# Optimization experiments

Hardware: AMD Instinct MI355X
Metric: run time of the kernel (lower is better)

## Reference

```python
import jax, jax.numpy as jnp
import numpy as np

L, D, H, DK, DV, VOCAB, PAD = 6, 512, 8, 64, 64, 10000, 0
B, S, NR = 32, 64, 196

def setup_inputs() -> dict:
    key = jax.random.key(0)
    ks = jax.random.split(key, 16)
    sd = 0.02
    emb = jax.random.normal(ks[0], (VOCAB, D), jnp.float32) * sd
    emb = emb.at[PAD].set(0.0)  # padding_idx row is zero in torch Embedding
    def w(k, shape):
        return jax.random.normal(k, shape, jnp.float32) * sd
    return {
        "x": jax.random.randint(ks[1], (B, S), 0, VOCAB),
        "K": jax.random.normal(ks[2], (B, NR, D), jnp.float32),
        "V": jax.random.normal(ks[3], (B, NR, D), jnp.float32),
        "g": jax.random.normal(ks[4], (B, D), jnp.float32),
        "batch_size": B,
        "emb": emb,
        "Wq_s": w(ks[5], (L, D, H * DK)),
        "Wk_s": w(ks[6], (L, D, H * DK)),
        "Wv_s": w(ks[7], (L, D, H * DV)),
        "Wo_s": w(ks[8], (L, H * DV, D)),
        "Wq_c": w(ks[9], (L, D, H * DK)),
        "Wg_c": w(ks[10], (L, D, H * DK)),
        "Wk_c": w(ks[11], (L, D, H * DK)),
        "Wv_c": w(ks[12], (L, D, H * DV)),
        "Wo_c": w(ks[13], (L, H * DV, D)),
        "Wf": w(ks[14], (D, VOCAB)),
        "bf": jnp.zeros((VOCAB,), jnp.float32),
    }

def positional_encoding(seq_len, d_model):
    pos = jnp.arange(seq_len, dtype=jnp.float32)[:, None]          # [S,1]
    j = jnp.arange(d_model // 2, dtype=jnp.float32)[None, :]       # [1,D/2]
    ang = pos / jnp.power(10000.0, 2.0 * j / d_model)              # [S,D/2]
    pe = jnp.stack([jnp.sin(ang), jnp.cos(ang)], axis=-1)          # [S,D/2,2]
    return pe.reshape(seq_len, d_model)

def attend(q, k, v, mask):
    # q:[B,Sq,H,DK] k:[B,Sk,H,DK] v:[B,Sk,H,DV]
    scores = jnp.einsum('bqhd,bkhd->bhqk', q, k) / jnp.sqrt(jnp.float32(DK))
    if mask is not None:
        scores = jnp.where(mask[None, None], scores, jnp.finfo(scores.dtype).min)
    attn = jax.nn.softmax(scores, axis=-1)
    return jnp.einsum('bhqk,bkhd->bqhd', attn, v)

def reference(x, K, V, g, batch_size, emb, Wq_s, Wk_s, Wv_s, Wo_s,
              Wq_c, Wg_c, Wk_c, Wv_c, Wo_c, Wf, bf):
    b, s = x.shape
    out = emb[x] + positional_encoding(s, D)[None]                 # [B,S,D]
    mask = jnp.tril(jnp.ones((s, s), bool))                        # causal: True = attend
    for l in range(L):
        # masked multi-head self-attention
        q = (out @ Wq_s[l]).reshape(b, s, H, DK)
        k = (out @ Wk_s[l]).reshape(b, s, H, DK)
        v = (out @ Wv_s[l]).reshape(b, s, H, DV)
        out = attend(q, k, v, mask).reshape(b, s, H * DV) @ Wo_s[l]
        # global-adaptive cross-attention: query conditioned on global feature g
        q = (out @ Wq_c[l] + (g @ Wg_c[l])[:, None, :]).reshape(b, s, H, DK)
        kk = (K @ Wk_c[l]).reshape(b, NR, H, DK)
        vv = (V @ Wv_c[l]).reshape(b, NR, H, DV)
        out = attend(q, kk, vv, None).reshape(b, s, H * DV) @ Wo_c[l]
    return jax.nn.softmax(out @ Wf + bf, axis=-1)                  # [B,S,VOCAB]
```

## Files before the change

### kernel.cpp

```cpp
#include <hip/hip_runtime.h>
#include <math.h>


#define S2 (512*512)
typedef unsigned short ushort_t;
typedef unsigned int u32;
typedef __attribute__((ext_vector_type(8))) short short8;
typedef __attribute__((ext_vector_type(4))) float f32x4;

__device__ __forceinline__ ushort_t f2b(float f) {
    union { float f; u32 u; } v; v.f = f;
    u32 r = (v.u + 0x7fffu + ((v.u >> 16) & 1u)) >> 16;
    return (ushort_t)r;
}
__device__ __forceinline__ float b2f(ushort_t u) {
    union { u32 u; float f; } v; v.u = ((u32)u) << 16; return v.f;
}
__device__ __forceinline__ void glds16(const void* g, void* l) {
    __builtin_amdgcn_global_load_lds((const __attribute__((address_space(1))) u32*)g,
                                     (__attribute__((address_space(3))) u32*)l,
                                     16, 0, 0);
}
__device__ __forceinline__ f32x4 mfma16(short8 a, short8 b, f32x4 c) {
    return __builtin_amdgcn_mfma_f32_16x16x32_bf16(a, b, c, 0, 0, 0);
}

__device__ __forceinline__ void tile128(
    const ushort_t* __restrict__ A, const ushort_t* __restrict__ B,
    ushort_t* __restrict__ Cp, int N, int K, const float* __restrict__ biasc,
    int m0, int n0, ushort_t* As, ushort_t* Bs, ushort_t* Cs)
{
    int t = threadIdx.x;
    int sr = t >> 2, sk = (t & 3) * 8;
    int wv = t >> 6, lane = t & 63;
    int wr = (wv >> 1) * 64, wc = (wv & 1) * 64;
    int lr = lane & 15, lq = lane >> 4;

    f32x4 acc[4][4];
#pragma unroll
    for (int i = 0; i < 4; ++i)
#pragma unroll
        for (int j = 0; j < 4; ++j) acc[i][j] = (f32x4){0.f, 0.f, 0.f, 0.f};

    for (int k0 = 0; k0 < K; k0 += 32) {
        glds16(A + (long)(m0 + sr) * K + k0 + sk,      (void*)(As + t * 8));
        glds16(A + (long)(m0 + sr + 64) * K + k0 + sk, (void*)(As + (t + 256) * 8));
        glds16(B + (long)(n0 + sr) * K + k0 + sk,      (void*)(Bs + t * 8));
        glds16(B + (long)(n0 + sr + 64) * K + k0 + sk, (void*)(Bs + (t + 256) * 8));
        __syncthreads();
        short8 af[4], bfr[4];
#pragma unroll
        for (int i = 0; i < 4; ++i)
            af[i] = *(const short8*)&As[(wr + i * 16 + lr) * 32 + lq * 8];
#pragma unroll
        for (int j = 0; j < 4; ++j)
            bfr[j] = *(const short8*)&Bs[(wc + j * 16 + lr) * 32 + lq * 8];
#pragma unroll
        for (int i = 0; i < 4; ++i)
#pragma unroll
            for (int j = 0; j < 4; ++j)
                acc[i][j] = mfma16(af[i], bfr[j], acc[i][j]);
        __syncthreads();
    }

    ushort_t* Cw = Cs + wv * 16 * 80;
#pragma unroll
    for (int i = 0; i < 4; ++i) {
#pragma unroll
        for (int j = 0; j < 4; ++j) {
            int colg = n0 + wc + j * 16 + lr;
            float bb = (biasc && colg < N) ? biasc[colg] : 0.f;
#pragma unroll
            for (int r = 0; r < 4; ++r)
                Cw[(lq * 4 + r) * 80 + j * 16 + lr] = f2b(acc[i][j][r] + bb);
        }
        __syncthreads();
#pragma unroll
        for (int rr = 0; rr < 2; ++rr) {
            int c = lane + 64 * rr;
            int row = c >> 3, g8 = c & 7;
            uint4 u = *(const uint4*)&Cw[row * 80 + g8 * 8];
            int colg = n0 + wc + g8 * 8;
            int rowg = m0 + wr + i * 16 + row;
            if (colg < N) *(uint4*)&Cp[(long)rowg * N + colg] = u;
        }
        __syncthreads();
    }
}

__global__ __launch_bounds__(256) void gemm_bt(
    const ushort_t* __restrict__ A, const ushort_t* __restrict__ B,
    ushort_t* __restrict__ C, int N, int K, const float* __restrict__ biasc)
{
    __shared__ ushort_t As[128 * 32], Bs[128 * 32];
    __shared__ __align__(16) ushort_t Cs[4 * 16 * 80];
    tile128(A, B, C, N, K, biasc, blockIdx.y * 128, blockIdx.x * 128, As, Bs, Cs);
}

__global__ __launch_bounds__(256) void fusew(
    const ushort_t* __restrict__ W8t, const ushort_t* __restrict__ Wo_sp,
    const ushort_t* __restrict__ Wo_cp, ushort_t* __restrict__ Fqc_t,
    ushort_t* __restrict__ Fqkv_t)
{
    __shared__ ushort_t As[128 * 32], Bs[128 * 32];
    __shared__ __align__(16) ushort_t Cs[4 * 16 * 80];
    int z = blockIdx.z;
    const ushort_t *A, *B; ushort_t* C;
    if (z < 6)      { A = W8t + (long)(24 + z) * S2; B = Wo_sp + (long)z * S2; C = Fqc_t + (long)z * S2; }
    else { int zz = z - 6, l = zz / 3, m = zz % 3;
           A = W8t + (long)(m * 6 + l + 1) * S2; B = Wo_cp + (long)l * S2; C = Fqkv_t + (long)zz * S2; }
    tile128(A, B, C, 512, 512, nullptr, blockIdx.y * 128, blockIdx.x * 128, As, Bs, Cs);
}

__global__ __launch_bounds__(256) void prep(
    const int* __restrict__ x, const float* __restrict__ emb,
    const float* __restrict__ Wq_s, const float* __restrict__ Wk_s,
    const float* __restrict__ Wv_s, const float* __restrict__ Wo_s,
    const float* __restrict__ Wq_c, const float* __restrict__ Wg_c,
    const float* __restrict__ Wk_c, const float* __restrict__ Wv_c,
    const float* __restrict__ Wo_c, const float* __restrict__ Wf,
    const float* __restrict__ Kin, const float* __restrict__ Vin,
    const float* __restrict__ g,
    ushort_t* __restrict__ W8t, ushort_t* __restrict__ Wf_t,
    ushort_t* __restrict__ Wo_sp, ushort_t* __restrict__ Wo_cp,
    ushort_t* __restrict__ K_bf, ushort_t* __restrict__ V_bf,
    ushort_t* __restrict__ act0, float* __restrict__ gq)
{
    __shared__ float tile[2][64][65];
    int bid = blockIdx.x, t = threadIdx.x;
    if (bid < 1536) {
        int mat = bid >> 5, wsel = mat / 6, l = mat % 6;
        const float* src = (wsel == 0) ? Wq_s : (wsel == 1) ? Wk_s : (wsel == 2) ? Wv_s :
                           (wsel == 3) ? Wo_s : (wsel == 4) ? Wq_c : (wsel == 5) ? Wk_c :
                           (wsel == 6) ? Wv_c : Wo_c;
        src += (long)l * S2;
        ushort_t* dst = W8t + (long)mat * S2;
        ushort_t* plain = (wsel == 3) ? Wo_sp + (long)l * S2
                        : (wsel == 7) ? Wo_cp + (long)l * S2 : nullptr;
        int within = bid & 31;
        int n0 = (within & 7) * 64, kb = (within >> 3) * 128;
        int r0 = t >> 4, c4 = (t & 15) * 4;
        float4 v[2][4];
#pragma unroll
        for (int h2 = 0; h2 < 2; ++h2)
#pragma unroll
            for (int p = 0; p < 4; ++p)
                v[h2][p] = *(const float4*)(src + (long)(kb + h2 * 64 + p * 16 + r0) * 512 + n0 + c4);
#pragma unroll
        for (int h2 = 0; h2 < 2; ++h2)
#pragma unroll
            for (int p = 0; p < 4; ++p) {
                int r = p * 16 + r0;
                tile[h2][c4 + 0][r] = v[h2][p].x; tile[h2][c4 + 1][r] = v[h2][p].y;
                tile[h2][c4 + 2][r] = v[h2][p].z; tile[h2][c4 + 3][r] = v[h2][p].w;
            }
        if (plain) {
#pragma unroll
            for (int h2 = 0; h2 < 2; ++h2)
#pragma unroll
                for (int p = 0; p < 4; ++p) {
                    ushort4 w;
                    w.x = f2b(v[h2][p].x); w.y = f2b(v[h2][p].y);
                    w.z = f2b(v[h2][p].z); w.w = f2b(v[h2][p].w);
                    *(ushort4*)(plain + (long)(kb + h2 * 64 + p * 16 + r0) * 512 + n0 + c4) = w;
                }
        }
        __syncthreads();
#pragma unroll
        for (int h2 = 0; h2 < 2; ++h2)
#pragma unroll
            for (int q = 0; q < 2; ++q) {
                int nl = q * 32 + (t >> 3), k8 = (t & 7) * 8;
                short8 o;
#pragma unroll
                for (int u = 0; u < 8; ++u) o[u] = (short)f2b(tile[h2][nl][k8 + u]);
                *(short8*)(dst + (long)(n0 + nl) * 512 + kb + h2 * 64 + k8) = o;
            }
    } else if (bid < 2168) {
        int id = bid - 1536;
        int n0 = (id % 158) * 64, kb = (id / 158) * 128;
        int r0 = t >> 4, c4 = (t & 15) * 4;
        int n = n0 + c4;
        float4 v[2][4];
#pragma unroll
        for (int h2 = 0; h2 < 2; ++h2)
#pragma unroll
            for (int p = 0; p < 4; ++p) {
                const float* row = Wf + (long)(kb + h2 * 64 + p * 16 + r0) * 10000;
                float4 w;
                if (n + 3 < 10000) {
                    w = *(const float4*)(row + n);
                } else {
                    w.x = (n + 0 < 10000) ? row[n + 0] : 0.f;
                    w.y = (n + 1 < 10000) ? row[n + 1] : 0.f;
                    w.z = (n + 2 < 10000) ? row[n + 2] : 0.f;
                    w.w = (n + 3 < 10000) ? row[n + 3] : 0.f;
                }
                v[h2][p] = w;
            }
#pragma unroll
        for (int h2 = 0; h2 < 2; ++h2)
#pragma unroll
            for (int p = 0; p < 4; ++p) {
                int r = p * 16 + r0;
                tile[h2][c4 + 0][r] = v[h2][p].x; tile[h2][c4 + 1][r] = v[h2][p].y;
                tile[h2][c4 + 2][r] = v[h2][p].z; tile[h2][c4 + 3][r] = v[h2][p].w;
            }
        __syncthreads();
#pragma unroll
        for (int h2 = 0; h2 < 2; ++h2)
#pragma unroll
            for (int q = 0; q < 2; ++q) {
                int nl = q * 32 + (t >> 3), k8 = (t & 7) * 8;
                short8 o;
#pragma unroll
                for (int u = 0; u < 8; ++u) o[u] = (short)f2b(tile[h2][nl][k8 + u]);
                *(short8*)(Wf_t + (long)(n0 + nl) * 512 + kb + h2 * 64 + k8) = o;
            }
    } else if (bid < 2952) {
        int sec = bid - 2168;
        const float* s; ushort_t* o; long fbase;
        if (sec < 392) { s = Kin; o = K_bf; fbase = (long)sec * 2048; }
        else           { s = Vin; o = V_bf; fbase = (long)(sec - 392) * 2048; }
        float4 v[8];
#pragma unroll
        for (int u = 0; u < 8; ++u)
            v[u] = *(const float4*)(s + 4 * (fbase + t + 256 * u));
#pragma unroll
        for (int u = 0; u < 8; ++u) {
            long fi = fbase + t + 256 * u;
            ushort4 w;
            w.x = f2b(v[u].x); w.y = f2b(v[u].y); w.z = f2b(v[u].z); w.w = f2b(v[u].w);
            *(ushort4*)(o + 4 * fi) = w;
        }
    } else if (bid < 3464) {
        long i = (long)(bid - 2952) * 2048 + t * 8;
        long tok = i >> 9;
        int d8 = (int)(i & 511);
        int s = (int)(tok & 63);
        int id = x[tok];
        const float* erow = emb + (long)id * 512 + d8;
        float4 e0 = *(const float4*)(erow);
        float4 e1 = *(const float4*)(erow + 4);
        float ev[8] = {e0.x, e0.y, e0.z, e0.w, e1.x, e1.y, e1.z, e1.w};
        int j0 = d8 >> 1;
        float sf = (float)s;
        short8 o;
#pragma unroll
        for (int u = 0; u < 4; ++u) {
            float invf = expf(-0.035977892f * (float)(j0 + u));
            float ang = sf * invf;
            o[2 * u]     = (short)f2b(ev[2 * u]     + sinf(ang));
            o[2 * u + 1] = (short)f2b(ev[2 * u + 1] + cosf(ang));
        }
        *(short8*)(act0 + i) = o;
    } else {
        __shared__ float gs[512];
        int id = bid - 3464;
        int lb = id >> 1, half = id & 1;
        int l = lb >> 5, b = lb & 31;
        for (int i = t; i < 512; i += 256) gs[i] = g[b * 512 + i];
        __syncthreads();
        int o = half * 256 + t;
        const float* wcol = Wg_c + (long)l * S2 + o;
        float acc = 0.f;
#pragma unroll 8
        for (int i = 0; i < 512; ++i) acc += gs[i] * wcol[(long)i * 512];
        gq[((long)l * 32 + b) * 512 + o] = acc;
    }
}

__global__ __launch_bounds__(256, 1) void layer_self(
    const ushort_t* __restrict__ act,
    const ushort_t* __restrict__ Wq, const ushort_t* __restrict__ Wk,
    const ushort_t* __restrict__ Wv, ushort_t* __restrict__ attnout)
{
    __shared__ __align__(16) char smem[111616];
    ushort_t* Wst = (ushort_t*)smem;
    ushort_t* Qs  = (ushort_t*)(smem + 66560);
    ushort_t* Ks  = (ushort_t*)(smem + 75776);
    ushort_t* Vt  = (ushort_t*)(smem + 84992);
    float*    Ss  = (float*)(smem + 94208);

    int b = blockIdx.x >> 3, h = blockIdx.x & 7;
    int t = threadIdx.x, wv = t >> 6, lane = t & 63;
    int lr = lane & 15, lq = lane >> 4;
    const ushort_t* actb = act + (long)b * 64 * 512;

    for (int mat = 0; mat < 3; ++mat) {
        const ushort_t* W = ((mat == 0) ? Wq : (mat == 1) ? Wk : Wv) + h * 64 * 512;
        __syncthreads();
#pragma unroll
        for (int i = 0; i < 16; ++i) {
            int row = i * 4 + wv;
            glds16(W + row * 512 + lane * 8, Wst + row * 520 + lane * 8);
        }
        __syncthreads();
        f32x4 acc[4];
#pragma unroll
        for (int j = 0; j < 4; ++j) acc[j] = (f32x4){0.f, 0.f, 0.f, 0.f};
        const ushort_t* arow = actb + (wv * 16 + lr) * 512;
#pragma unroll 4
        for (int k = 0; k < 16; ++k) {
            short8 a = *(const short8*)(arow + k * 32 + lq * 8);
#pragma unroll
            for (int j = 0; j < 4; ++j) {
                short8 bb = *(const short8*)&Wst[(j * 16 + lr) * 520 + k * 32 + lq * 8];
                acc[j] = mfma16(a, bb, acc[j]);
            }
        }
        if (mat == 2) {
#pragma unroll
            for (int j = 0; j < 4; ++j)
#pragma unroll
                for (int r = 0; r < 4; ++r)
                    Vt[(j * 16 + lr) * 72 + wv * 16 + lq * 4 + r] = f2b(acc[j][r]);
        } else {
            ushort_t* Dst = (mat == 0) ? Qs : Ks;
#pragma unroll
            for (int j = 0; j < 4; ++j)
#pragma unroll
                for (int r = 0; r < 4; ++r)
                    Dst[(wv * 16 + lq * 4 + r) * 72 + j * 16 + lr] = f2b(acc[j][r]);
        }
    }
    __syncthreads();

    f32x4 sc[4];
#pragma unroll
    for (int j = 0; j < 4; ++j) sc[j] = (f32x4){0.f, 0.f, 0.f, 0.f};
#pragma unroll
    for (int k2 = 0; k2 < 2; ++k2) {
        short8 a = *(const short8*)&Qs[(wv * 16 + lr) * 72 + k2 * 32 + lq * 8];
#pragma unroll
        for (int j = 0; j < 4; ++j) {
            short8 bb = *(const short8*)&Ks[(j * 16 + lr) * 72 + k2 * 32 + lq * 8];
            sc[j] = mfma16(a, bb, sc[j]);
        }
    }
#pragma unroll
    for (int j = 0; j < 4; ++j)
#pragma unroll
        for (int r = 0; r < 4; ++r)
            Ss[(wv * 16 + lq * 4 + r) * 68 + j * 16 + lr] = sc[j][r];
    __syncthreads();

    for (int rr = 0; rr < 16; ++rr) {
        int r = wv * 16 + rr;
        float sv = (lane <= r) ? Ss[r * 68 + lane] * 0.125f : -INFINITY;
        float m = sv;
        for (int off = 32; off; off >>= 1) m = fmaxf(m, __shfl_xor(m, off));
        float p = __expf(sv - m);
        float su = p;
        for (int off = 32; off; off >>= 1) su += __shfl_xor(su, off);
        Qs[r * 72 + lane] = f2b(p / su);
    }
    __syncthreads();

    f32x4 ov[4];
#pragma unroll
    for (int j = 0; j < 4; ++j) ov[j] = (f32x4){0.f, 0.f, 0.f, 0.f};
#pragma unroll
    for (int k2 = 0; k2 < 2; ++k2) {
        short8 a = *(const short8*)&Qs[(wv * 16 + lr) * 72 + k2 * 32 + lq * 8];
#pragma unroll
        for (int j = 0; j < 4; ++j) {
            short8 bb = *(const short8*)&Vt[(j * 16 + lr) * 72 + k2 * 32 + lq * 8];
            ov[j] = mfma16(a, bb, ov[j]);
        }
    }
    long obase = ((long)b * 64) * 512 + h * 64;
#pragma unroll
    for (int j = 0; j < 4; ++j)
#pragma unroll
        for (int r = 0; r < 4; ++r)
            attnout[obase + (long)(wv * 16 + lq * 4 + r) * 512 + j * 16 + lr] = f2b(ov[j][r]);
}

__global__ __launch_bounds__(256, 1) void layer_cross(
    const ushort_t* __restrict__ attnout, const ushort_t* __restrict__ Kb,
    const ushort_t* __restrict__ Vb, const ushort_t* __restrict__ Fqc,
    const ushort_t* __restrict__ Wkc, const ushort_t* __restrict__ Wvc,
    const float* __restrict__ gql, ushort_t* __restrict__ crossout)
{
    __shared__ __align__(16) char smem[134400];
    ushort_t* Wst = (ushort_t*)smem;
    float*    Ss  = (float*)smem;
    ushort_t* Qs  = (ushort_t*)(smem + 66560);
    ushort_t* Kc  = (ushort_t*)(smem + 75776);
    ushort_t* Pb  = Kc;
    ushort_t* Vt  = (ushort_t*)(smem + 105728);

    int b = blockIdx.x >> 3, h = blockIdx.x & 7;
    int t = threadIdx.x, wv = t >> 6, lane = t & 63;
    int lr = lane & 15, lq = lane >> 4;
    const ushort_t* atb = attnout + (long)b * 64 * 512;
    const ushort_t* Kbb = Kb + (long)b * 196 * 512;
    const ushort_t* Vbb = Vb + (long)b * 196 * 512;

    {
        const ushort_t* W = Fqc + h * 64 * 512;
#pragma unroll
        for (int i = 0; i < 16; ++i) {
            int row = i * 4 + wv;
            glds16(W + row * 512 + lane * 8, Wst + row * 520 + lane * 8);
        }
        __syncthreads();
        f32x4 acc[4];
#pragma unroll
        for (int j = 0; j < 4; ++j) acc[j] = (f32x4){0.f, 0.f, 0.f, 0.f};
        const ushort_t* arow = atb + (wv * 16 + lr) * 512;
#pragma unroll 4
        for (int k = 0; k < 16; ++k) {
            short8 a = *(const short8*)(arow + k * 32 + lq * 8);
#pragma unroll
            for (int j = 0; j < 4; ++j) {
                short8 bb = *(const short8*)&Wst[(j * 16 + lr) * 520 + k * 32 + lq * 8];
                acc[j] = mfma16(a, bb, acc[j]);
            }
        }
#pragma unroll
        for (int j = 0; j < 4; ++j)
#pragma unroll
            for (int r = 0; r < 4; ++r) {
                int col = j * 16 + lr;
                Qs[(wv * 16 + lq * 4 + r) * 72 + col] =
                    f2b(acc[j][r] + gql[b * 512 + h * 64 + col]);
            }
    }
#pragma unroll
    for (int mat = 0; mat < 2; ++mat) {
        const ushort_t* W = ((mat == 0) ? Wkc : Wvc) + h * 64 * 512;
        const ushort_t* Src = (mat == 0) ? Kbb : Vbb;
        __syncthreads();
#pragma unroll
        for (int i = 0; i < 16; ++i) {
            int row = i * 4 + wv;
            glds16(W + row * 512 + lane * 8, Wst + row * 520 + lane * 8);
        }
        __syncthreads();
        for (int rt = wv; rt < 13; rt += 4) {
            f32x4 acc[4];
#pragma unroll
            for (int j = 0; j < 4; ++j) acc[j] = (f32x4){0.f, 0.f, 0.f, 0.f};
            const ushort_t* arow = Src + (long)(rt * 16 + lr) * 512;
#pragma unroll 4
            for (int k = 0; k < 16; ++k) {
                short8 a = *(const short8*)(arow + k * 32 + lq * 8);
#pragma unroll
                for (int j = 0; j < 4; ++j) {
                    short8 bb = *(const short8*)&Wst[(j * 16 + lr) * 520 + k * 32 + lq * 8];
                    acc[j] = mfma16(a, bb, acc[j]);
                }
            }
            if (mat == 0) {
#pragma unroll
                for (int j = 0; j < 4; ++j)
#pragma unroll
                    for (int r = 0; r < 4; ++r)
                        Kc[(rt * 16 + lq * 4 + r) * 72 + j * 16 + lr] = f2b(acc[j][r]);
            } else {
#pragma unroll
                for (int j = 0; j < 4; ++j)
#pragma unroll
                    for (int r = 0; r < 4; ++r)
                        Vt[(j * 16 + lr) * 224 + rt * 16 + lq * 4 + r] = f2b(acc[j][r]);
            }
        }
    }
    __syncthreads();
    for (int e = t; e < 64 * 28; e += 256) Vt[(e / 28) * 224 + 196 + (e % 28)] = 0;

    f32x4 sc[13];
#pragma unroll
    for (int ct = 0; ct < 13; ++ct) sc[ct] = (f32x4){0.f, 0.f, 0.f, 0.f};
#pragma unroll
    for (int k2 = 0; k2 < 2; ++k2) {
        short8 a = *(const short8*)&Qs[(wv * 16 + lr) * 72 + k2 * 32 + lq * 8];
#pragma unroll
        for (int ct = 0; ct < 13; ++ct) {
            short8 bb = *(const short8*)&Kc[(ct * 16 + lr) * 72 + k2 * 32 + lq * 8];
            sc[ct] = mfma16(a, bb, sc[ct]);
        }
    }
#pragma unroll
    for (int ct = 0; ct < 13; ++ct)
#pragma unroll
        for (int r = 0; r < 4; ++r)
            Ss[(wv * 16 + lq * 4 + r) * 216 + ct * 16 + lr] = sc[ct][r];
    __syncthreads();

    for (int rr = 0; rr < 16; ++rr) {
        int r = wv * 16 + rr;
        float v0 = Ss[r * 216 + lane] * 0.125f;
        float v1 = Ss[r * 216 + 64 + lane] * 0.125f;
        float v2 = Ss[r * 216 + 128 + lane] * 0.125f;
        float v3 = (lane < 4) ? Ss[r * 216 + 192 + lane] * 0.125f : -INFINITY;
        float m = fmaxf(fmaxf(v0, v1), fmaxf(v2, v3));
        for (int off = 32; off; off >>= 1) m = fmaxf(m, __shfl_xor(m, off));
        float e0 = __expf(v0 - m), e1 = __expf(v1 - m), e2 = __expf(v2 - m);
        float e3 = (lane < 4) ? __expf(v3 - m) : 0.f;
        float su = e0 + e1 + e2 + e3;
        for (int off = 32; off; off >>= 1) su += __shfl_xor(su, off);
        float inv = 1.f / su;
        Pb[r * 224 + lane]       = f2b(e0 * inv);
        Pb[r * 224 + 64 + lane]  = f2b(e1 * inv);
        Pb[r * 224 + 128 + lane] = f2b(e2 * inv);
        if (lane < 4)  Pb[r * 224 + 192 + lane] = f2b(e3 * inv);
        if (lane < 28) Pb[r * 224 + 196 + lane] = 0;
    }
    __syncthreads();

    f32x4 ov[4];
#pragma unroll
    for (int j = 0; j < 4; ++j) ov[j] = (f32x4){0.f, 0.f, 0.f, 0.f};
#pragma unroll
    for (int k2 = 0; k2 < 7; ++k2) {
        short8 a = *(const short8*)&Pb[(wv * 16 + lr) * 224 + k2 * 32 + lq * 8];
#pragma unroll
        for (int j = 0; j < 4; ++j) {
            short8 bb = *(const short8*)&Vt[(j * 16 + lr) * 224 + k2 * 32 + lq * 8];
            ov[j] = mfma16(a, bb, ov[j]);
        }
    }
    long obase = ((long)b * 64) * 512 + h * 64;
#pragma unroll
    for (int j = 0; j < 4; ++j)
#pragma unroll
        for (int r = 0; r < 4; ++r)
            crossout[obase + (long)(wv * 16 + lq * 4 + r) * 512 + j * 16 + lr] = f2b(ov[j][r]);
}

__global__ __launch_bounds__(256) void softmax_bf(const ushort_t* __restrict__ lg,
                                                  float* __restrict__ out)
{
    __shared__ float red[8];
    long row = blockIdx.x;
    const ushort_t* p = lg + row * 10000L;
    float* po = out + row * 10000L;
    int t = threadIdx.x;
    int w = t >> 6, lane = t & 63;
    float vals[40];
    float mx = -INFINITY;
#pragma unroll
    for (int ii = 0; ii < 40; ++ii) {
        int c = t + (ii << 8);
        if (c < 10000) { float v = b2f(p[c]); vals[ii] = v; mx = fmaxf(mx, v); }
        else vals[ii] = -INFINITY;
    }
    for (int off = 32; off; off >>= 1) mx = fmaxf(mx, __shfl_xor(mx, off));
    if (lane == 0) red[w] = mx;
    __syncthreads();
    mx = fmaxf(fmaxf(red[0], red[1]), fmaxf(red[2], red[3]));
    float s = 0.f;
#pragma unroll
    for (int ii = 0; ii < 40; ++ii) {
        float e = __expf(vals[ii] - mx);
        vals[ii] = e;
        s += e;
    }
    for (int off = 32; off; off >>= 1) s += __shfl_xor(s, off);
    if (lane == 0) red[4 + w] = s;
    __syncthreads();
    s = red[4] + red[5] + red[6] + red[7];
    float inv = 1.0f / s;
#pragma unroll
    for (int ii = 0; ii < 40; ++ii) {
        int c = t + (ii << 8);
        if (c < 10000) po[c] = vals[ii] * inv;
    }
}

extern "C" void kernel_launch(void* const* d_in, const int* in_sizes, int n_in,
                              void* d_out, int out_size, void* d_ws, size_t ws_size,
                              hipStream_t stream)
{
    const int*   x    = (const int*)d_in[0];
    const float* Kin  = (const float*)d_in[1];
    const float* Vin  = (const float*)d_in[2];
    const float* g    = (const float*)d_in[3];
    const float* emb  = (const float*)d_in[5];
    const float* Wq_s = (const float*)d_in[6];
    const float* Wk_s = (const float*)d_in[7];
    const float* Wv_s = (const float*)d_in[8];
    const float* Wo_s = (const float*)d_in[9];
    const float* Wq_c = (const float*)d_in[10];
    const float* Wg_c = (const float*)d_in[11];
    const float* Wk_c = (const float*)d_in[12];
    const float* Wv_c = (const float*)d_in[13];
    const float* Wo_c = (const float*)d_in[14];
    const float* Wf   = (const float*)d_in[15];
    const float* bf   = (const float*)d_in[16];
    float* out = (float*)d_out;

    float* gq = (float*)d_ws;
    ushort_t* act0     = (ushort_t*)(gq + 98304);
    ushort_t* crossout = act0 + 1048576;
    ushort_t* attnout  = crossout + 1048576;
    ushort_t* K_bf     = attnout + 1048576;
    ushort_t* V_bf     = K_bf + 3211264;
    ushort_t* W8t      = V_bf + 3211264;
    ushort_t* Wf_t     = W8t + 48L * S2;
    ushort_t* Wo_sp    = Wf_t + 5177344;
    ushort_t* Wo_cp    = Wo_sp + 6L * S2;
    ushort_t* Fqc_t    = Wo_cp + 6L * S2;
    ushort_t* Fqkv_t   = Fqc_t + 6L * S2;
    ushort_t* Wfin_t   = Fqkv_t + 15L * S2;
    ushort_t* logits   = W8t;

    prep<<<3848, 256, 0, stream>>>(x, emb, Wq_s, Wk_s, Wv_s, Wo_s, Wq_c, Wg_c,
                                   Wk_c, Wv_c, Wo_c, Wf, Kin, Vin, g,
                                   W8t, Wf_t, Wo_sp, Wo_cp, K_bf, V_bf, act0, gq);
    fusew<<<dim3(4, 4, 21), 256, 0, stream>>>(W8t, Wo_sp, Wo_cp, Fqc_t, Fqkv_t);
    gemm_bt<<<dim3(4, 79, 1), 256, 0, stream>>>(Wf_t, Wo_cp + 5L * S2, Wfin_t,
                                                512, 512, nullptr);

    for (int l = 0; l < 6; ++l) {
        const ushort_t *A, *Bq, *Bk, *Bv;
        if (l == 0) {
            A = act0;
            Bq = W8t + 0L * 6 * S2; Bk = W8t + 1L * 6 * S2; Bv = W8t + 2L * 6 * S2;
        } else {
            A = crossout;
            Bq = Fqkv_t + (long)((l - 1) * 3) * S2;
            Bk = Bq + S2; Bv = Bq + 2 * S2;
        }
        layer_self<<<256, 256, 0, stream>>>(A, Bq, Bk, Bv, attnout);
        layer_cross<<<256, 256, 0, stream>>>(attnout, K_bf, V_bf,
                                             Fqc_t + (long)l * S2,
                                             W8t + (long)(5 * 6 + l) * S2,
                                             W8t + (long)(6 * 6 + l) * S2,
                                             gq + (long)l * 16384, crossout);
    }

    gemm_bt<<<dim3(79, 16, 1), 256, 0, stream>>>(crossout, Wfin_t, logits,
                                                 10000, 512, bf);
    softmax_bf<<<2048, 256, 0, stream>>>(logits, out);
}
```

Measured before the change: 739.9 us.

## Precompute cross-attention K/V projections for all layers in one batched GEMM

Adds a kcv_gemm kernel that projects the bf16 K and V inputs through every layer's cross-attention Wk/Wv in one large launch before the layer loop. A new layer_cross_pre kernel then reads these precomputed per-head slices instead of doing the projection inside each block. The old per-block kernel redid the projection once per (batch, head) block per layer, and the batched tiled GEMM replaces that with a high-throughput tiled pass. The cost is a large extra workspace (about 77 MB of projected K/V), and the new path only runs when ws_size is large enough, otherwise the old kernel is used. The final softmax also switches to 16-byte vector loads and float4 stores.

```diff
diff --git a/kernel.cpp b/kernel.cpp
--- a/kernel.cpp
+++ b/kernel.cpp
@@ -109,6 +109,19 @@
     if (z < 6)      { A = W8t + (long)(24 + z) * S2; B = Wo_sp + (long)z * S2; C = Fqc_t + (long)z * S2; }
     else { int zz = z - 6, l = zz / 3, m = zz % 3;
            A = W8t + (long)(m * 6 + l + 1) * S2; B = Wo_cp + (long)l * S2; C = Fqkv_t + (long)zz * S2; }
+    tile128(A, B, C, 512, 512, nullptr, blockIdx.y * 128, blockIdx.x * 128, As, Bs, Cs);
+}
+
+__global__ __launch_bounds__(256) void kcv_gemm(
+    const ushort_t* __restrict__ Kb, const ushort_t* __restrict__ Vb,
+    const ushort_t* __restrict__ W8t, ushort_t* __restrict__ kcv)
+{
+    __shared__ ushort_t As[128 * 32], Bs[128 * 32];
+    __shared__ __align__(16) ushort_t Cs[4 * 16 * 80];
+    int z = blockIdx.z, l = z >> 1, isv = z & 1;
+    const ushort_t* A = isv ? Vb : Kb;
+    const ushort_t* B = W8t + (long)(30 + isv * 6 + l) * S2;
+    ushort_t* C = kcv + (long)z * 3211264;
     tile128(A, B, C, 512, 512, nullptr, blockIdx.y * 128, blockIdx.x * 128, As, Bs, Cs);
 }
 
@@ -531,6 +544,134 @@
             crossout[obase + (long)(wv * 16 + lq * 4 + r) * 512 + j * 16 + lr] = f2b(ov[j][r]);
 }
 
+__global__ __launch_bounds__(256, 1) void layer_cross_pre(
+    const ushort_t* __restrict__ attnout, const ushort_t* __restrict__ kcl,
+    const ushort_t* __restrict__ vcl, const ushort_t* __restrict__ Fqc,
+    const float* __restrict__ gql, ushort_t* __restrict__ crossout)
+{
+    __shared__ __align__(16) char smem[134400];
+    ushort_t* Wst = (ushort_t*)smem;
+    float*    Ss  = (float*)smem;
+    ushort_t* Qs  = (ushort_t*)(smem + 66560);
+    ushort_t* Kc  = (ushort_t*)(smem + 75776);
+    ushort_t* Pb  = Kc;
+    ushort_t* Vt  = (ushort_t*)(smem + 105728);
+
+    int b = blockIdx.x >> 3, h = blockIdx.x & 7;
+    int t = threadIdx.x, wv = t >> 6, lane = t & 63;
+    int lr = lane & 15, lq = lane >> 4;
+    const ushort_t* atb = attnout + (long)b * 64 * 512;
+
+    {
+        const ushort_t* W = Fqc + h * 64 * 512;
+#pragma unroll
+        for (int i = 0; i < 16; ++i) {
+            int row = i * 4 + wv;
+            glds16(W + row * 512 + lane * 8, Wst + row * 520 + lane * 8);
+        }
+        __syncthreads();
+        f32x4 acc[4];
+#pragma unroll
+        for (int j = 0; j < 4; ++j) acc[j] = (f32x4){0.f, 0.f, 0.f, 0.f};
+        const ushort_t* arow = atb + (wv * 16 + lr) * 512;
+#pragma unroll 4
+        for (int k = 0; k < 16; ++k) {
+            short8 a = *(const short8*)(arow + k * 32 + lq * 8);
+#pragma unroll
+            for (int j = 0; j < 4; ++j) {
+                short8 bb = *(const short8*)&Wst[(j * 16 + lr) * 520 + k * 32 + lq * 8];
+                acc[j] = mfma16(a, bb, acc[j]);
+            }
+        }
+#pragma unroll
+        for (int j = 0; j < 4; ++j)
+#pragma unroll
+            for (int r = 0; r < 4; ++r) {
+                int col = j * 16 + lr;
+                Qs[(wv * 16 + lq * 4 + r) * 72 + col] =
+                    f2b(acc[j][r] + gql[b * 512 + h * 64 + col]);
+            }
+    }
+
+    {
+        const ushort_t* kr = kcl + ((long)b * 196) * 512 + h * 64;
+        for (int idx = t; idx < 208 * 8; idx += 256) {
+            int key = idx >> 3, d8 = (idx & 7) * 8;
+            short8 v = (short8){0, 0, 0, 0, 0, 0, 0, 0};
+            if (key < 196) v = *(const short8*)(kr + (long)key * 512 + d8);
+            *(short8*)&Kc[key * 72 + d8] = v;
+        }
+        const ushort_t* vrp = vcl + ((long)b * 196) * 512 + h * 64;
+        for (int idx = t; idx < 196 * 8; idx += 256) {
+            int key = idx >> 3, d8 = (idx & 7) * 8;
+            short8 v = *(const short8*)(vrp + (long)key * 512 + d8);
+#pragma unroll
+            for (int u = 0; u < 8; ++u) Vt[(d8 + u) * 224 + key] = v[u];
+        }
+        for (int e = t; e < 64 * 28; e += 256) Vt[(e / 28) * 224 + 196 + (e % 28)] = 0;
+    }
+    __syncthreads();
+
+    f32x4 sc[13];
+#pragma unroll
+    for (int ct = 0; ct < 13; ++ct) sc[ct] = (f32x4){0.f, 0.f, 0.f, 0.f};
+#pragma unroll
+    for (int k2 = 0; k2 < 2; ++k2) {
+        short8 a = *(const short8*)&Qs[(wv * 16 + lr) * 72 + k2 * 32 + lq * 8];
+#pragma unroll
+        for (int ct = 0; ct < 13; ++ct) {
+            short8 bb = *(const short8*)&Kc[(ct * 16 + lr) * 72 + k2 * 32 + lq * 8];
+            sc[ct] = mfma16(a, bb, sc[ct]);
+        }
+    }
+#pragma unroll
+    for (int ct = 0; ct < 13; ++ct)
+#pragma unroll
+        for (int r = 0; r < 4; ++r)
+            Ss[(wv * 16 + lq * 4 + r) * 216 + ct * 16 + lr] = sc[ct][r];
+    __syncthreads();
+
+    for (int rr = 0; rr < 16; ++rr) {
+        int r = wv * 16 + rr;
+        float v0 = Ss[r * 216 + lane] * 0.125f;
+        float v1 = Ss[r * 216 + 64 + lane] * 0.125f;
+        float v2 = Ss[r * 216 + 128 + lane] * 0.125f;
+        float v3 = (lane < 4) ? Ss[r * 216 + 192 + lane] * 0.125f : -INFINITY;
+        float m = fmaxf(fmaxf(v0, v1), fmaxf(v2, v3));
+        for (int off = 32; off; off >>= 1) m = fmaxf(m, __shfl_xor(m, off));
+        float e0 = __expf(v0 - m), e1 = __expf(v1 - m), e2 = __expf(v2 - m);
+        float e3 = (lane < 4) ? __expf(v3 - m) : 0.f;
+        float su = e0 + e1 + e2 + e3;
+        for (int off = 32; off; off >>= 1) su += __shfl_xor(su, off);
+        float inv = 1.f / su;
+        Pb[r * 224 + lane]       = f2b(e0 * inv);
+        Pb[r * 224 + 64 + lane]  = f2b(e1 * inv);
+        Pb[r * 224 + 128 + lane] = f2b(e2 * inv);
+        if (lane < 4)  Pb[r * 224 + 192 + lane] = f2b(e3 * inv);
+        if (lane < 28) Pb[r * 224 + 196 + lane] = 0;
+    }
+    __syncthreads();
+
+    f32x4 ov[4];
+#pragma unroll
+    for (int j = 0; j < 4; ++j) ov[j] = (f32x4){0.f, 0.f, 0.f, 0.f};
+#pragma unroll
+    for (int k2 = 0; k2 < 7; ++k2) {
+        short8 a = *(const short8*)&Pb[(wv * 16 + lr) * 224 + k2 * 32 + lq * 8];
+#pragma unroll
+        for (int j = 0; j < 4; ++j) {
+            short8 bb = *(const short8*)&Vt[(j * 16 + lr) * 224 + k2 * 32 + lq * 8];
+            ov[j] = mfma16(a, bb, ov[j]);
+        }
+    }
+    long obase = ((long)b * 64) * 512 + h * 64;
+#pragma unroll
+    for (int j = 0; j < 4; ++j)
+#pragma unroll
+        for (int r = 0; r < 4; ++r)
+            crossout[obase + (long)(wv * 16 + lq * 4 + r) * 512 + j * 16 + lr] = f2b(ov[j][r]);
+}
+
 __global__ __launch_bounds__(256) void softmax_bf(const ushort_t* __restrict__ lg,
                                                   float* __restrict__ out)
 {
@@ -543,10 +684,20 @@
     float vals[40];
     float mx = -INFINITY;
 #pragma unroll
-    for (int ii = 0; ii < 40; ++ii) {
-        int c = t + (ii << 8);
-        if (c < 10000) { float v = b2f(p[c]); vals[ii] = v; mx = fmaxf(mx, v); }
-        else vals[ii] = -INFINITY;
+    for (int i = 0; i < 5; ++i) {
+        int vi = t + (i << 8);
+        if (vi < 1250) {
+            short8 v = *(const short8*)(p + vi * 8);
+#pragma unroll
+            for (int u = 0; u < 8; ++u) {
+                float f = b2f((ushort_t)v[u]);
+                vals[i * 8 + u] = f;
+                mx = fmaxf(mx, f);
+            }
+        } else {
+#pragma unroll
+            for (int u = 0; u < 8; ++u) vals[i * 8 + u] = -INFINITY;
+        }
     }
     for (int off = 32; off; off >>= 1) mx = fmaxf(mx, __shfl_xor(mx, off));
     if (lane == 0) red[w] = mx;
@@ -565,9 +716,19 @@
     s = red[4] + red[5] + red[6] + red[7];
     float inv = 1.0f / s;
 #pragma unroll
-    for (int ii = 0; ii < 40; ++ii) {
-        int c = t + (ii << 8);
-        if (c < 10000) po[c] = vals[ii] * inv;
+    for (int i = 0; i < 5; ++i) {
+        int vi = t + (i << 8);
+        if (vi < 1250) {
+#pragma unroll
+            for (int u4 = 0; u4 < 2; ++u4) {
+                float4 o;
+                o.x = vals[i * 8 + u4 * 4 + 0] * inv;
+                o.y = vals[i * 8 + u4 * 4 + 1] * inv;
+                o.z = vals[i * 8 + u4 * 4 + 2] * inv;
+                o.w = vals[i * 8 + u4 * 4 + 3] * inv;
+                *(float4*)(po + vi * 8 + u4 * 4) = o;
+            }
+        }
     }
 }
 
@@ -606,7 +767,10 @@
     ushort_t* Fqc_t    = Wo_cp + 6L * S2;
     ushort_t* Fqkv_t   = Fqc_t + 6L * S2;
     ushort_t* Wfin_t   = Fqkv_t + 15L * S2;
+    ushort_t* kcv      = Wfin_t + 5177344;
     ushort_t* logits   = W8t;
+
+    int use_pre = (ws_size >= 159776768ULL) ? 1 : 0;
 
     prep<<<3848, 256, 0, stream>>>(x, emb, Wq_s, Wk_s, Wv_s, Wo_s, Wq_c, Wg_c,
                                    Wk_c, Wv_c, Wo_c, Wf, Kin, Vin, g,
@@ -614,6 +778,8 @@
     fusew<<<dim3(4, 4, 21), 256, 0, stream>>>(W8t, Wo_sp, Wo_cp, Fqc_t, Fqkv_t);
     gemm_bt<<<dim3(4, 79, 1), 256, 0, stream>>>(Wf_t, Wo_cp + 5L * S2, Wfin_t,
                                                 512, 512, nullptr);
+    if (use_pre)
+        kcv_gemm<<<dim3(4, 49, 12), 256, 0, stream>>>(K_bf, V_bf, W8t, kcv);
 
     for (int l = 0; l < 6; ++l) {
         const ushort_t *A, *Bq, *Bk, *Bv;
@@ -626,11 +792,18 @@
             Bk = Bq + S2; Bv = Bq + 2 * S2;
         }
         layer_self<<<256, 256, 0, stream>>>(A, Bq, Bk, Bv, attnout);
-        layer_cross<<<256, 256, 0, stream>>>(attnout, K_bf, V_bf,
-                                             Fqc_t + (long)l * S2,
-                                             W8t + (long)(5 * 6 + l) * S2,
-                                             W8t + (long)(6 * 6 + l) * S2,
-                                             gq + (long)l * 16384, crossout);
+        if (use_pre)
+            layer_cross_pre<<<256, 256, 0, stream>>>(attnout,
+                                                     kcv + (long)(l * 2) * 3211264,
+                                                     kcv + (long)(l * 2 + 1) * 3211264,
+                                                     Fqc_t + (long)l * S2,
+                                                     gq + (long)l * 16384, crossout);
+        else
+            layer_cross<<<256, 256, 0, stream>>>(attnout, K_bf, V_bf,
+                                                 Fqc_t + (long)l * S2,
+                                                 W8t + (long)(5 * 6 + l) * S2,
+                                                 W8t + (long)(6 * 6 + l) * S2,
+                                                 gq + (long)l * 16384, crossout);
     }
 
     gemm_bt<<<dim3(79, 16, 1), 256, 0, stream>>>(crossout, Wfin_t, logits,
```

After: 655.1 us. 11.5% less time.
